# Performance work log

Measured on AMD Instinct MI355X. Metric: run time of the kernel, lower is better.

The kernel has to match this reference:

```python
import jax, jax.numpy as jnp
import numpy as np
import math

DIM = 2048
N_HEADS = 32
N_KV_HEADS = 8
HEAD_DIM = DIM // N_HEADS  # 64
N_REP = N_HEADS // N_KV_HEADS
B, S = 2, 2048


def _rope(x, cos, sin):
    # x: [B, S, H, Hd]; cos/sin: [S, Hd//2]
    xr = x[..., 0::2]
    xi = x[..., 1::2]
    c = cos[None, :, None, :]
    s = sin[None, :, None, :]
    or_ = xr * c - xi * s
    oi_ = xr * s + xi * c
    return jnp.stack([or_, oi_], axis=-1).reshape(x.shape)


def setup_inputs() -> dict:
    key = jax.random.key(0)
    ks = jax.random.split(key, 8)
    x = jax.random.normal(ks[0], (B, S, DIM), dtype=jnp.float32)
    # standard RoPE frequency tables
    inv_freq = 1.0 / (10000.0 ** (np.arange(0, HEAD_DIM, 2, dtype=np.float32) / HEAD_DIM))
    t = np.arange(S, dtype=np.float32)
    freqs = np.outer(t, inv_freq)  # [S, HEAD_DIM//2]
    freqs_cos = jnp.asarray(np.cos(freqs))
    freqs_sin = jnp.asarray(np.sin(freqs))
    attn_mask = jnp.zeros((S, S), dtype=jnp.float32)
    sc = 0.02
    wq = jax.random.normal(ks[1], (DIM, N_HEADS * HEAD_DIM), dtype=jnp.float32) * sc
    wk = jax.random.normal(ks[2], (DIM, N_KV_HEADS * HEAD_DIM), dtype=jnp.float32) * sc
    wv = jax.random.normal(ks[3], (DIM, N_KV_HEADS * HEAD_DIM), dtype=jnp.float32) * sc
    wo = jax.random.normal(ks[4], (DIM, DIM), dtype=jnp.float32) * sc
    return {"x": x, "freqs_cos": freqs_cos, "freqs_sin": freqs_sin,
            "attn_mask": attn_mask, "wq": wq, "wk": wk, "wv": wv, "wo": wo}


def reference(x, freqs_cos, freqs_sin, attn_mask, wq, wk, wv, wo):
    bsz, seqlen, _ = x.shape
    xq = (x @ wq).reshape(bsz, seqlen, N_HEADS, HEAD_DIM)
    xk = (x @ wk).reshape(bsz, seqlen, N_KV_HEADS, HEAD_DIM)
    xv = (x @ wv).reshape(bsz, seqlen, N_KV_HEADS, HEAD_DIM)
    xq = _rope(xq, freqs_cos, freqs_sin)
    xk = _rope(xk, freqs_cos, freqs_sin)
    # GQA repeat: [B,S,Hkv,Hd] -> [B,S,H,Hd]
    xk = jnp.repeat(xk, N_REP, axis=2)
    xv = jnp.repeat(xv, N_REP, axis=2)
    xq = xq.swapaxes(1, 2)  # [B,H,S,Hd]
    xk = xk.swapaxes(1, 2)
    xv = xv.swapaxes(1, 2)
    scores = jnp.einsum('bhqd,bhkd->bhqk', xq, xk) / math.sqrt(HEAD_DIM)
    scores = scores + attn_mask[None, None, :seqlen, :seqlen]
    probs = jax.nn.softmax(scores, axis=-1)
    out = jnp.einsum('bhqk,bhkd->bhqd', probs, xv)
    out = out.swapaxes(1, 2).reshape(bsz, seqlen, -1)
    return out @ wo
```

## Files before the change

### kernel.cpp

```cpp
#include <hip/hip_runtime.h>

typedef unsigned short u16;
typedef __bf16 bf16x8 __attribute__((ext_vector_type(8)));
typedef float f32x4 __attribute__((ext_vector_type(4)));
typedef float f32x16 __attribute__((ext_vector_type(16)));
typedef unsigned short u16x4 __attribute__((ext_vector_type(4)));
typedef unsigned int u32x4 __attribute__((ext_vector_type(4)));

typedef __attribute__((address_space(1))) const unsigned int* gas_t;
typedef __attribute__((address_space(3))) unsigned int* las_t;

__device__ __forceinline__ void gload16(const void* gsrc, void* ldst) {
  __builtin_amdgcn_global_load_lds((gas_t)gsrc, (las_t)ldst, 16, 0, 0);
}

__device__ __forceinline__ u16 f2bf(float f) {
  unsigned u = __builtin_bit_cast(unsigned, f);
  unsigned r = u + 0x7fffu + ((u >> 16) & 1u);
  return (u16)(r >> 16);
}
__device__ __forceinline__ float bf2f(u16 h) {
  unsigned u = ((unsigned)h) << 16;
  return __builtin_bit_cast(float, u);
}
__device__ __forceinline__ unsigned cvtpk(float lo, float hi) {
  unsigned r;
  asm("v_cvt_pk_bf16_f32 %0, %1, %2" : "=v"(r) : "v"(lo), "v"(hi));
  return r;
}
__device__ __forceinline__ float fexp2(float x) {
  return __builtin_amdgcn_exp2f(x);
}

__global__ __launch_bounds__(256) void cvt_x(const float* __restrict__ x, u16* __restrict__ xb) {
  int i = blockIdx.x * 256 + threadIdx.x;
  f32x4 v = ((const f32x4*)x)[i];
  u16x4 o = { f2bf(v[0]), f2bf(v[1]), f2bf(v[2]), f2bf(v[3]) };
  ((u16x4*)xb)[i] = o;
}

__global__ __launch_bounds__(256) void transpose_cvt(const float* __restrict__ in, u16* __restrict__ out,
                                                     int K, int N) {
  __shared__ float tile[32][33];
  int n0 = blockIdx.x * 32, k0 = blockIdx.y * 32;
  int tx = threadIdx.x, ty = threadIdx.y;
#pragma unroll
  for (int i = 0; i < 4; ++i)
    tile[ty + i * 8][tx] = in[(size_t)(k0 + ty + i * 8) * N + n0 + tx];
  __syncthreads();
#pragma unroll
  for (int i = 0; i < 4; ++i)
    out[(size_t)(n0 + ty + i * 8) * K + k0 + tx] = f2bf(tile[tx][ty + i * 8]);
}

template <int OUTBF>
__global__ __launch_bounds__(256) void gemm_bt(const u16* __restrict__ A, const u16* __restrict__ Bt,
                                               void* __restrict__ Cout, int M, int N, int K) {
  __shared__ u16 As[128 * 64];
  __shared__ u16 Bs[128 * 64];
  const int tid = threadIdx.x;
  const int w = tid >> 6, l = tid & 63, lg = l >> 4, lr = l & 15;
  const int m0 = blockIdx.y * 128, n0 = blockIdx.x * 128;
  const int wr = w >> 1, wc = w & 1;

  size_t srcA[4], srcB[4];
  int ldst[4];
#pragma unroll
  for (int j = 0; j < 4; ++j) {
    int c = j * 256 + tid;
    int row = c >> 3, kb = (c & 7) ^ (row & 7);
    srcA[j] = (size_t)(m0 + row) * K + kb * 8;
    srcB[j] = (size_t)(n0 + row) * K + kb * 8;
    ldst[j] = (j * 256 + w * 64) * 8;
  }

  const int lx = lr & 7;
  int aoff[2][4], boff[2][4];
#pragma unroll
  for (int kk = 0; kk < 2; ++kk) {
#pragma unroll
    for (int m = 0; m < 4; ++m)
      aoff[kk][m] = (wr * 64 + m * 16 + lr) * 128 + ((((kk << 2) | lg) ^ lx) << 4);
#pragma unroll
    for (int n = 0; n < 4; ++n)
      boff[kk][n] = (wc * 64 + n * 16 + lr) * 128 + ((((kk << 2) | lg) ^ lx) << 4);
  }

  f32x4 acc[4][4];
#pragma unroll
  for (int m = 0; m < 4; ++m)
#pragma unroll
    for (int n = 0; n < 4; ++n) acc[m][n] = (f32x4){0.f, 0.f, 0.f, 0.f};

  for (int k0 = 0; k0 < K; k0 += 64) {
    __syncthreads();
#pragma unroll
    for (int j = 0; j < 4; ++j) {
      gload16(A + k0 + srcA[j], &As[ldst[j]]);
      gload16(Bt + k0 + srcB[j], &Bs[ldst[j]]);
    }
    __syncthreads();
#pragma unroll
    for (int kk = 0; kk < 2; ++kk) {
      bf16x8 af[4], bf[4];
#pragma unroll
      for (int m = 0; m < 4; ++m)
        af[m] = *(const bf16x8*)((const char*)As + aoff[kk][m]);
#pragma unroll
      for (int n = 0; n < 4; ++n)
        bf[n] = *(const bf16x8*)((const char*)Bs + boff[kk][n]);
      __builtin_amdgcn_s_setprio(1);
#pragma unroll
      for (int m = 0; m < 4; ++m)
#pragma unroll
        for (int n = 0; n < 4; ++n)
          acc[m][n] = __builtin_amdgcn_mfma_f32_16x16x32_bf16(af[m], bf[n], acc[m][n], 0, 0, 0);
      __builtin_amdgcn_s_setprio(0);
    }
  }
#pragma unroll
  for (int m = 0; m < 4; ++m)
#pragma unroll
    for (int n = 0; n < 4; ++n)
#pragma unroll
      for (int r = 0; r < 4; ++r) {
        int row = m0 + wr * 64 + m * 16 + lg * 4 + r;
        int col = n0 + wc * 64 + n * 16 + lr;
        float v = acc[m][n][r];
        if (OUTBF)
          ((u16*)Cout)[(size_t)row * N + col] = f2bf(v);
        else
          ((float*)Cout)[(size_t)row * N + col] = v;
      }
}

__global__ __launch_bounds__(256) void rope_kernel(const u16* __restrict__ qkv, const float* __restrict__ fcos,
                                                   const float* __restrict__ fsin, u16* __restrict__ dst,
                                                   int nhs , int col0) {
  int idx = blockIdx.x * 256 + threadIdx.x;
  int p = idx & 31;
  int h = (idx >> 5) & ((1 << nhs) - 1);
  int t = idx >> (5 + nhs);
  int s = t & 2047, b = t >> 11;
  unsigned v = *(const unsigned*)(qkv + (size_t)t * 3072 + col0 + h * 64 + 2 * p);
  float xr = bf2f((u16)(v & 0xffff)), xi = bf2f((u16)(v >> 16));
  float c = fcos[s * 32 + p], sn = fsin[s * 32 + p];
  float orr = xr * c - xi * sn;
  float oii = xr * sn + xi * c;
  unsigned o = (unsigned)f2bf(orr) | ((unsigned)f2bf(oii) << 16);
  *(unsigned*)(dst + (((size_t)((b << nhs) + h) * 2048 + s) * 64 + 2 * p)) = o;
}

__global__ __launch_bounds__(256) void vtrans(const u16* __restrict__ qkv, u16* __restrict__ vT) {
  __shared__ u16 tile[32][33];
  int c0 = blockIdx.x * 32, t0 = blockIdx.y * 32;
  int tx = threadIdx.x, ty = threadIdx.y;
#pragma unroll
  for (int i = 0; i < 4; ++i)
    tile[ty + i * 8][tx] = qkv[(size_t)(t0 + ty + i * 8) * 3072 + 2560 + c0 + tx];
  __syncthreads();
#pragma unroll
  for (int i = 0; i < 4; ++i) {
    int c = c0 + ty + i * 8;
    int tok = t0 + tx;
    int ts = (tok & ~15) | (tok & 3) | ((tok & 4) << 1) | ((tok & 8) >> 1);
    vT[((size_t)((tok >> 11) * 8 + (c >> 6)) * 64 + (c & 63)) * 2048 + (ts & 2047)] = tile[tx][ty + i * 8];
  }
}

__global__ __launch_bounds__(256) void mask_flags(const float* __restrict__ mask, unsigned* __restrict__ Fl) {
  int qt = blockIdx.x, kt = blockIdx.y;
  int t = threadIdx.x;
  int row = qt * 128 + (t >> 1);
  const f32x4* p = (const f32x4*)(mask + (size_t)row * 2048 + kt * 64 + (t & 1) * 32);
  bool any = false;
#pragma unroll
  for (int j = 0; j < 8; ++j) {
    f32x4 v = p[j];
    any |= (v[0] != 0.f) | (v[1] != 0.f) | (v[2] != 0.f) | (v[3] != 0.f);
  }
  if (__any(any) && (t & 63) == 0) atomicOr(&Fl[qt], 1u << kt);
}

__global__ __launch_bounds__(256, 4) void attn(const u16* __restrict__ Q, const u16* __restrict__ Kb,
                                               const u16* __restrict__ Vt, const float* __restrict__ mask,
                                               const unsigned* __restrict__ Fl, u16* __restrict__ Ao) {
  __shared__ u16 Ks[2][4096];
  __shared__ u16 Vs[2][4096];
  __shared__ float cbuf[128];
  const int bid = blockIdx.x;
  const int qt = bid & 15, h = (bid >> 4) & 31, b = bid >> 9;
  const int kv = h >> 2;
  const int tid = threadIdx.x, w = tid >> 6, l = tid & 63;
  const int lq = l & 31, hi = l >> 5;

  const float C = 0.125f * 1.44269504088896f;

  const u16* Qb = Q + ((size_t)((b * 32 + h) * 2048 + qt * 128 + w * 32 + lq)) * 64;
  bf16x8 qf[4];
#pragma unroll
  for (int t = 0; t < 4; ++t)
    qf[t] = *(const bf16x8*)(Qb + t * 16 + hi * 8);

  const u16* Ksrc = Kb + (size_t)(b * 8 + kv) * 2048 * 64;
  const u16* Vsrc = Vt + (size_t)(b * 8 + kv) * 64 * 2048;
  const float* Mrow = mask + (size_t)(qt * 128 + w * 32 + lq) * 2048;
  const unsigned flagbits = Fl[qt];

  const int lx = lq & 7;
  int koff[8];
#pragma unroll
  for (int ks = 0; ks < 2; ++ks)
#pragma unroll
    for (int t = 0; t < 4; ++t)
      koff[ks * 4 + t] = (lq + 32 * ks) * 128 + ((((t << 1) + hi) ^ lx) << 4);
  int voff[8];
#pragma unroll
  for (int ks = 0; ks < 2; ++ks)
#pragma unroll
    for (int t = 0; t < 2; ++t)
#pragma unroll
      for (int dblk = 0; dblk < 2; ++dblk)
        voff[(ks * 2 + t) * 2 + dblk] =
            (lq + 32 * dblk) * 128 + ((((ks << 2) + (t << 1) + hi) ^ lx) << 4);

  size_t kgoff[2], vgoff[2];
  int ldso[2];
#pragma unroll
  for (int j = 0; j < 2; ++j) {
    int c = w * 64 + j * 256 + l;
    int row = c >> 3;
    int sc_ = ((c & 7) ^ (row & 7)) * 8;
    kgoff[j] = (size_t)row * 64 + sc_;
    vgoff[j] = (size_t)row * 2048 + sc_;
    ldso[j] = (w * 64 + j * 256) * 8;
  }

  f32x16 o0, o1, zacc;
#pragma unroll
  for (int i = 0; i < 16; ++i) { o0[i] = 0.f; o1[i] = 0.f; zacc[i] = 0.f; }
  float mrun2 = 0.f, lrun = 0.f;

  auto stage = [&](int kt2, int bu2) {
#pragma unroll
    for (int j = 0; j < 2; ++j) {
      gload16(Ksrc + (size_t)kt2 * 4096 + kgoff[j], &Ks[bu2][ldso[j]]);
      gload16(Vsrc + (size_t)kt2 * 64 + vgoff[j], &Vs[bu2][ldso[j]]);
    }
  };

  stage(0, 0);
  __syncthreads();

  for (int kt = 0; kt < 32; ++kt) {
    const int bu = kt & 1;
    if (kt < 31) stage(kt + 1, bu ^ 1);
    const char* KL = (const char*)Ks[bu];
    const char* VL = (const char*)Vs[bu];
    const bool havemask = (flagbits >> kt) & 1;

#pragma unroll
    for (int ks = 0; ks < 2; ++ks) {
      __builtin_amdgcn_s_setprio(1);
      bf16x8 kf = *(const bf16x8*)(KL + koff[ks * 4]);
      f32x16 a = __builtin_amdgcn_mfma_f32_32x32x16_bf16(kf, qf[0], zacc, 0, 0, 0);
#pragma unroll
      for (int t = 1; t < 4; ++t) {
        kf = *(const bf16x8*)(KL + koff[ks * 4 + t]);
        a = __builtin_amdgcn_mfma_f32_32x32x16_bf16(kf, qf[t], a, 0, 0, 0);
      }
      __builtin_amdgcn_s_setprio(0);

      if (havemask) {
#pragma unroll
        for (int g = 0; g < 4; ++g) {
          f32x4 mk = *(const f32x4*)(Mrow + kt * 64 + ks * 32 + g * 8 + hi * 4);
#pragma unroll
          for (int i = 0; i < 4; ++i) a[g * 4 + i] = fmaf(mk[i], 8.0f, a[g * 4 + i]);
        }
      }

      float ps0 = 0.f, ps1 = 0.f, ps2 = 0.f, ps3 = 0.f;
#pragma unroll
      for (int i = 0; i < 16; i += 4) {
        float p0 = fexp2(fmaf(a[i], C, -mrun2));
        float p1 = fexp2(fmaf(a[i + 1], C, -mrun2));
        float p2 = fexp2(fmaf(a[i + 2], C, -mrun2));
        float p3 = fexp2(fmaf(a[i + 3], C, -mrun2));
        a[i] = p0; a[i + 1] = p1; a[i + 2] = p2; a[i + 3] = p3;
        ps0 += p0; ps1 += p1; ps2 += p2; ps3 += p3;
      }
      lrun += (ps0 + ps1) + (ps2 + ps3);

      unsigned uu0 = cvtpk(a[0], a[1]);
      unsigned uu1 = cvtpk(a[2], a[3]);
      unsigned uu2 = cvtpk(a[4], a[5]);
      unsigned uu3 = cvtpk(a[6], a[7]);
      unsigned uu4 = cvtpk(a[8], a[9]);
      unsigned uu5 = cvtpk(a[10], a[11]);
      unsigned uu6 = cvtpk(a[12], a[13]);
      unsigned uu7 = cvtpk(a[14], a[15]);
      __builtin_amdgcn_s_setprio(1);
#pragma unroll
      for (int t = 0; t < 2; ++t) {
        u32x4 wv_;
        if (t == 0) wv_ = (u32x4){uu0, uu1, uu2, uu3};
        else        wv_ = (u32x4){uu4, uu5, uu6, uu7};
        bf16x8 pa = __builtin_bit_cast(bf16x8, wv_);
#pragma unroll
        for (int dblk = 0; dblk < 2; ++dblk) {
          bf16x8 vfrag = *(const bf16x8*)(VL + voff[(ks * 2 + t) * 2 + dblk]);
          if (dblk == 0) o0 = __builtin_amdgcn_mfma_f32_32x32x16_bf16(pa, vfrag, o0, 0, 0, 0);
          else           o1 = __builtin_amdgcn_mfma_f32_32x32x16_bf16(pa, vfrag, o1, 0, 0, 0);
        }
      }
      __builtin_amdgcn_s_setprio(0);
    }

    if (__builtin_expect(__any(lrun > 1.0e27f), 0)) {
      const float DS = 5.421010862427522e-20f;
      mrun2 += 64.0f;
      lrun *= DS;
#pragma unroll
      for (int r = 0; r < 16; ++r) { o0[r] *= DS; o1[r] *= DS; }
    }

    __syncthreads();
  }

  lrun += __shfl_xor(lrun, 32);
  if (l < 32) cbuf[(w << 5) + l] = 1.0f / lrun;
  asm volatile("s_waitcnt lgkmcnt(0)" ::: "memory");
#pragma unroll
  for (int r = 0; r < 16; ++r) {
    int oq = (r & 3) + 8 * (r >> 2) + 4 * hi;
    float inv = cbuf[(w << 5) + oq];
    int srow = qt * 128 + w * 32 + oq;
    size_t tok = (size_t)(b * 2048 + srow);
    Ao[tok * 2048 + h * 64 + lq]      = f2bf(o0[r] * inv);
    Ao[tok * 2048 + h * 64 + 32 + lq] = f2bf(o1[r] * inv);
  }
}

extern "C" void kernel_launch(void* const* d_in, const int* in_sizes, int n_in,
                              void* d_out, int out_size, void* d_ws, size_t ws_size,
                              hipStream_t stream) {
  const float* x    = (const float*)d_in[0];
  const float* fcos = (const float*)d_in[1];
  const float* fsin = (const float*)d_in[2];
  const float* mask = (const float*)d_in[3];
  const float* wq   = (const float*)d_in[4];
  const float* wk   = (const float*)d_in[5];
  const float* wv   = (const float*)d_in[6];
  const float* wo   = (const float*)d_in[7];
  float* out = (float*)d_out;

  u16* ws  = (u16*)d_ws;
  u16* xb  = ws;
  u16* wT  = ws + 8388608;
  u16* qkv = ws + 14680064;
  u16* qb  = ws + 27262976;
  u16* kb  = ws + 35651584;
  u16* vT  = ws + 37748736;
  unsigned* Fl = (unsigned*)qkv;

  cvt_x<<<8192, 256, 0, stream>>>(x, xb);
  transpose_cvt<<<dim3(64, 64), dim3(32, 8), 0, stream>>>(wq, wT, 2048, 2048);
  transpose_cvt<<<dim3(16, 64), dim3(32, 8), 0, stream>>>(wk, wT + (size_t)2048 * 2048, 2048, 512);
  transpose_cvt<<<dim3(16, 64), dim3(32, 8), 0, stream>>>(wv, wT + (size_t)2560 * 2048, 2048, 512);
  gemm_bt<1><<<dim3(24, 32), 256, 0, stream>>>(xb, wT, qkv, 4096, 3072, 2048);
  transpose_cvt<<<dim3(64, 64), dim3(32, 8), 0, stream>>>(wo, wT, 2048, 2048);
  rope_kernel<<<16384, 256, 0, stream>>>(qkv, fcos, fsin, qb, 5, 0);
  rope_kernel<<<4096, 256, 0, stream>>>(qkv, fcos, fsin, kb, 3, 2048);
  vtrans<<<dim3(16, 128), dim3(32, 8), 0, stream>>>(qkv, vT);
  hipMemsetAsync(Fl, 0, 16 * sizeof(unsigned), stream);
  mask_flags<<<dim3(16, 32), 256, 0, stream>>>(mask, Fl);
  attn<<<1024, 256, 0, stream>>>(qb, kb, vT, mask, Fl, xb);
  gemm_bt<0><<<dim3(16, 32), 256, 0, stream>>>(xb, wT, out, 4096, 2048, 2048);
}
```

Measured before the change: 227.6 us.

## Fuse RoPE and softmax scale into QKV GEMM epilogue, drop rope kernels

```diff
diff --git a/kernel.cpp b/kernel.cpp
--- a/kernel.cpp
+++ b/kernel.cpp
@@ -32,6 +32,9 @@
   return __builtin_amdgcn_exp2f(x);
 }
 
+#define QSCALE 0.1803368801111204f
+#define L2E    1.44269504088896f
+
 __global__ __launch_bounds__(256) void cvt_x(const float* __restrict__ x, u16* __restrict__ xb) {
   int i = blockIdx.x * 256 + threadIdx.x;
   f32x4 v = ((const f32x4*)x)[i];
@@ -53,9 +56,11 @@
     out[(size_t)(n0 + ty + i * 8) * K + k0 + tx] = f2bf(tile[tx][ty + i * 8]);
 }
 
-template <int OUTBF>
+template <int MODE>
 __global__ __launch_bounds__(256) void gemm_bt(const u16* __restrict__ A, const u16* __restrict__ Bt,
-                                               void* __restrict__ Cout, int M, int N, int K) {
+                                               void* __restrict__ Cout, int M, int N, int K,
+                                               const float* __restrict__ fcos, const float* __restrict__ fsin,
+                                               u16* __restrict__ qdst, u16* __restrict__ kdst) {
   __shared__ u16 As[128 * 64];
   __shared__ u16 Bs[128 * 64];
   const int tid = threadIdx.x;
@@ -118,6 +123,35 @@
       __builtin_amdgcn_s_setprio(0);
     }
   }
+
+  if (MODE == 1 && n0 < 2560) {
+    const bool isQ = (n0 < 2048);
+#pragma unroll
+    for (int m = 0; m < 4; ++m)
+#pragma unroll
+      for (int n = 0; n < 4; ++n)
+#pragma unroll
+        for (int r = 0; r < 4; ++r) {
+          int row = m0 + wr * 64 + m * 16 + lg * 4 + r;
+          int col = n0 + wc * 64 + n * 16 + lr;
+          float v = acc[m][n][r];
+          float pv = __shfl_xor(v, 1);
+          int st = row & 2047, bb = row >> 11;
+          int p = (col & 63) >> 1;
+          float cc = fcos[st * 32 + p], sn = fsin[st * 32 + p];
+          float outv = ((lr & 1) == 0) ? (v * cc - pv * sn)
+                                       : (pv * sn + v * cc);
+          if (isQ) {
+            int hh = col >> 6;
+            qdst[((size_t)(bb * 32 + hh) * 2048 + st) * 64 + (col & 63)] = f2bf(outv * QSCALE);
+          } else {
+            int hh = (col - 2048) >> 6;
+            kdst[((size_t)(bb * 8 + hh) * 2048 + st) * 64 + (col & 63)] = f2bf(outv);
+          }
+        }
+    return;
+  }
+
 #pragma unroll
   for (int m = 0; m < 4; ++m)
 #pragma unroll
@@ -127,28 +161,11 @@
         int row = m0 + wr * 64 + m * 16 + lg * 4 + r;
         int col = n0 + wc * 64 + n * 16 + lr;
         float v = acc[m][n][r];
-        if (OUTBF)
+        if (MODE == 1)
           ((u16*)Cout)[(size_t)row * N + col] = f2bf(v);
         else
           ((float*)Cout)[(size_t)row * N + col] = v;
       }
-}
-
-__global__ __launch_bounds__(256) void rope_kernel(const u16* __restrict__ qkv, const float* __restrict__ fcos,
-                                                   const float* __restrict__ fsin, u16* __restrict__ dst,
-                                                   int nhs , int col0) {
-  int idx = blockIdx.x * 256 + threadIdx.x;
-  int p = idx & 31;
-  int h = (idx >> 5) & ((1 << nhs) - 1);
-  int t = idx >> (5 + nhs);
-  int s = t & 2047, b = t >> 11;
-  unsigned v = *(const unsigned*)(qkv + (size_t)t * 3072 + col0 + h * 64 + 2 * p);
-  float xr = bf2f((u16)(v & 0xffff)), xi = bf2f((u16)(v >> 16));
-  float c = fcos[s * 32 + p], sn = fsin[s * 32 + p];
-  float orr = xr * c - xi * sn;
-  float oii = xr * sn + xi * c;
-  unsigned o = (unsigned)f2bf(orr) | ((unsigned)f2bf(oii) << 16);
-  *(unsigned*)(dst + (((size_t)((b << nhs) + h) * 2048 + s) * 64 + 2 * p)) = o;
 }
 
 __global__ __launch_bounds__(256) void vtrans(const u16* __restrict__ qkv, u16* __restrict__ vT) {
@@ -194,8 +211,6 @@
   const int tid = threadIdx.x, w = tid >> 6, l = tid & 63;
   const int lq = l & 31, hi = l >> 5;
 
-  const float C = 0.125f * 1.44269504088896f;
-
   const u16* Qb = Q + ((size_t)((b * 32 + h) * 2048 + qt * 128 + w * 32 + lq)) * 64;
   bf16x8 qf[4];
 #pragma unroll
@@ -276,19 +291,31 @@
         for (int g = 0; g < 4; ++g) {
           f32x4 mk = *(const f32x4*)(Mrow + kt * 64 + ks * 32 + g * 8 + hi * 4);
 #pragma unroll
-          for (int i = 0; i < 4; ++i) a[g * 4 + i] = fmaf(mk[i], 8.0f, a[g * 4 + i]);
+          for (int i = 0; i < 4; ++i) a[g * 4 + i] = fmaf(mk[i], L2E, a[g * 4 + i]);
         }
       }
 
       float ps0 = 0.f, ps1 = 0.f, ps2 = 0.f, ps3 = 0.f;
-#pragma unroll
-      for (int i = 0; i < 16; i += 4) {
-        float p0 = fexp2(fmaf(a[i], C, -mrun2));
-        float p1 = fexp2(fmaf(a[i + 1], C, -mrun2));
-        float p2 = fexp2(fmaf(a[i + 2], C, -mrun2));
-        float p3 = fexp2(fmaf(a[i + 3], C, -mrun2));
-        a[i] = p0; a[i + 1] = p1; a[i + 2] = p2; a[i + 3] = p3;
-        ps0 += p0; ps1 += p1; ps2 += p2; ps3 += p3;
+      if (mrun2 == 0.f) {
+#pragma unroll
+        for (int i = 0; i < 16; i += 4) {
+          float p0 = fexp2(a[i]);
+          float p1 = fexp2(a[i + 1]);
+          float p2 = fexp2(a[i + 2]);
+          float p3 = fexp2(a[i + 3]);
+          a[i] = p0; a[i + 1] = p1; a[i + 2] = p2; a[i + 3] = p3;
+          ps0 += p0; ps1 += p1; ps2 += p2; ps3 += p3;
+        }
+      } else {
+#pragma unroll
+        for (int i = 0; i < 16; i += 4) {
+          float p0 = fexp2(a[i] - mrun2);
+          float p1 = fexp2(a[i + 1] - mrun2);
+          float p2 = fexp2(a[i + 2] - mrun2);
+          float p3 = fexp2(a[i + 3] - mrun2);
+          a[i] = p0; a[i + 1] = p1; a[i + 2] = p2; a[i + 3] = p3;
+          ps0 += p0; ps1 += p1; ps2 += p2; ps3 += p3;
+        }
       }
       lrun += (ps0 + ps1) + (ps2 + ps3);
 
@@ -368,13 +395,11 @@
   transpose_cvt<<<dim3(64, 64), dim3(32, 8), 0, stream>>>(wq, wT, 2048, 2048);
   transpose_cvt<<<dim3(16, 64), dim3(32, 8), 0, stream>>>(wk, wT + (size_t)2048 * 2048, 2048, 512);
   transpose_cvt<<<dim3(16, 64), dim3(32, 8), 0, stream>>>(wv, wT + (size_t)2560 * 2048, 2048, 512);
-  gemm_bt<1><<<dim3(24, 32), 256, 0, stream>>>(xb, wT, qkv, 4096, 3072, 2048);
+  gemm_bt<1><<<dim3(24, 32), 256, 0, stream>>>(xb, wT, qkv, 4096, 3072, 2048, fcos, fsin, qb, kb);
   transpose_cvt<<<dim3(64, 64), dim3(32, 8), 0, stream>>>(wo, wT, 2048, 2048);
-  rope_kernel<<<16384, 256, 0, stream>>>(qkv, fcos, fsin, qb, 5, 0);
-  rope_kernel<<<4096, 256, 0, stream>>>(qkv, fcos, fsin, kb, 3, 2048);
   vtrans<<<dim3(16, 128), dim3(32, 8), 0, stream>>>(qkv, vT);
   hipMemsetAsync(Fl, 0, 16 * sizeof(unsigned), stream);
   mask_flags<<<dim3(16, 32), 256, 0, stream>>>(mask, Fl);
   attn<<<1024, 256, 0, stream>>>(qb, kb, vT, mask, Fl, xb);
-  gemm_bt<0><<<dim3(16, 32), 256, 0, stream>>>(xb, wT, out, 4096, 2048, 2048);
-}
+  gemm_bt<0><<<dim3(16, 32), 256, 0, stream>>>(xb, wT, out, 4096, 2048, 2048, nullptr, nullptr, nullptr, nullptr);
+}
```

Measured after the change: 250.6 us. +10.1%, slower.
